# Kernel optimization log

Hardware: AMD Instinct MI355X
Metric: run time of the kernel (lower is better)

## Reference

```python
import jax, jax.numpy as jnp
import numpy as np

N = 256          # num agents
HID = 128        # hidden_dim
ACT = 5          # action_dim
NH = 4           # num_heads
D = HID + 16     # concat_hidden_dim = 144
E = D * NH       # mha embed dim = 576
HD = D           # per-head dim = E // NH = 144
OBS_RX, OBS_RY = 4, 2   # obs_r from fov_size=(9,5)
GRID = 40


def setup_inputs() -> dict:
    key = jax.random.key(0)
    ks = jax.random.split(key, 24)
    g = lambda k, shape, s: (jax.random.normal(k, shape, dtype=jnp.float32) * s)
    inp = {
        "hidden_state_n": g(ks[0], (N, HID), 1.0),
        "action_n": g(ks[1], (N, HID), 1.0),
        "state_n": jax.random.randint(ks[2], (N, 2), 0, GRID, dtype=jnp.int32),
        # obs encoder
        "W_enc": g(ks[3], (HID, 16), HID ** -0.5), "b_enc": jnp.zeros((16,), jnp.float32),
        # MHABlock outer projections
        "Wq": g(ks[4], (D, E), D ** -0.5), "bq": jnp.zeros((E,), jnp.float32),
        "Wk": g(ks[5], (D, E), D ** -0.5), "bk": jnp.zeros((E,), jnp.float32),
        "Wv": g(ks[6], (D, E), D ** -0.5), "bv": jnp.zeros((E,), jnp.float32),
        # nn.MultiheadAttention internal in/out projections
        "Wiq": g(ks[7], (E, E), E ** -0.5), "biq": jnp.zeros((E,), jnp.float32),
        "Wik": g(ks[8], (E, E), E ** -0.5), "bik": jnp.zeros((E,), jnp.float32),
        "Wiv": g(ks[9], (E, E), E ** -0.5), "biv": jnp.zeros((E,), jnp.float32),
        "Wo_proj": g(ks[10], (E, E), E ** -0.5), "bo_proj": jnp.zeros((E,), jnp.float32),
        "W_O": g(ks[11], (E, D), E ** -0.5),  # no bias
        # dueling decoders
        "W_val": g(ks[12], (D, 1), D ** -0.5), "b_val": jnp.zeros((1,), jnp.float32),
        "W_adv": g(ks[13], (D, ACT), D ** -0.5), "b_adv": jnp.zeros((ACT,), jnp.float32),
    }
    return inp


def reference(hidden_state_n, action_n, W_enc, b_enc, Wq, bq, Wk, bk, Wv, bv,
              Wiq, biq, Wik, bik, Wiv, biv, Wo_proj, bo_proj, W_O,
              W_val, b_val, W_adv, b_adv, state_n):
    n = hidden_state_n.shape[0]
    # observed_agents[i] = {j > i : |x_i-x_j|<=rx and |y_i-y_j|<=ry}
    pos = state_n.astype(jnp.int32)
    dx = jnp.abs(pos[:, None, 0] - pos[None, :, 0])
    dy = jnp.abs(pos[:, None, 1] - pos[None, :, 1])
    upper = jnp.arange(n)[None, :] > jnp.arange(n)[:, None]
    mask = (dx <= OBS_RX) & (dy <= OBS_RY) & upper            # [N,N], mask[i,j]: j observed by i

    # per-neighbor feature c_j = concat(obs_encoder(h_j), a_j)  -> [N, D]
    obs = hidden_state_n @ W_enc + b_enc                       # [N,16]
    C = jnp.concatenate([obs, action_n], axis=-1)              # [N,D]

    # MHABlock: outer Q/K/V projections then nn.MultiheadAttention
    q = (C @ Wq + bq) @ Wiq + biq                              # [N,E]
    k = (C @ Wk + bk) @ Wik + bik
    v = (C @ Wv + bv) @ Wiv + biv
    q2 = q.reshape(n, NH, HD)
    k2 = k.reshape(n, NH, HD)
    v2 = v.reshape(n, NH, HD)

    scale = 1.0 / np.sqrt(HD).astype(np.float32)
    S = jnp.einsum("jhd,khd->hjk", q2, k2) * scale             # [H,N,N] shared across agents

    pair = (mask[:, None, :, None] & mask[:, None, None, :])   # [N,1,Nq,Nk]
    logits = jnp.where(pair, S[None, :, :, :], -1e9)           # [N,H,N,N]
    m = jnp.max(logits, axis=-1, keepdims=True)
    p = jnp.exp(logits - m) * pair.astype(logits.dtype)
    attn = p / jnp.maximum(p.sum(axis=-1, keepdims=True), 1e-9)

    ctx = jnp.einsum("ihjk,khd->ijhd", attn, v2).reshape(n, n, E)  # [N,Nq,E]
    out = (ctx @ Wo_proj + bo_proj) @ W_O                          # [N,Nq,D]

    # sum over the (masked) neighbor/query axis -> per-agent h_i
    h = jnp.sum(out * mask[:, :, None].astype(out.dtype), axis=1)  # [N,D]

    V = h @ W_val + b_val                                          # [N,1]
    A = h @ W_adv + b_adv                                          # [N,ACT]
    Q = V + A - jnp.mean(A, axis=-1, keepdims=True)                # dueling Q
    return Q
```

## Files before the change

kernel.cpp:

```cpp
#include <hip/hip_runtime.h>

#define NAG 256
#define HID 128
#define ACT 5
#define NH 4
#define DD 144
#define EE 576
#define HDIM 144
#define CMAX 20

__device__ __forceinline__ void prod_tile24(
    const float* __restrict__ A, const float* __restrict__ W,
    float* __restrict__ out, int rowbase, int colbase, int N,
    int tid, float* __restrict__ sm)
{
    const int LDA = 580;
    float* As = sm;
    for (int idx = tid; idx < 24 * 144; idx += 256) {
        int r = idx / 144, c = idx % 144;
        *((float4*)&As[r * LDA + c * 4]) =
            *(const float4*)(A + (size_t)(rowbase + r) * 576 + c * 4);
    }
    __syncthreads();
    const int wave = tid >> 6, lane = tid & 63;
    const int colg = colbase + lane;
    const int colc = (colg < N) ? colg : (N - 1);
    const float* Wp = W + (size_t)(wave * 144) * N + colc;
    float acc[24] = {};
    float wv[24], wn[24];
    #pragma unroll
    for (int j = 0; j < 24; ++j) wv[j] = Wp[(size_t)j * N];
    for (int gi = 0; gi < 6; ++gi) {
        if (gi + 1 < 6) {
            const float* Wn = Wp + (size_t)(gi + 1) * 24 * N;
            #pragma unroll
            for (int j = 0; j < 24; ++j) wn[j] = Wn[(size_t)j * N];
        }
        const int kb = wave * 144 + gi * 24;
        #pragma unroll
        for (int j4 = 0; j4 < 6; ++j4) {
            #pragma unroll
            for (int r = 0; r < 24; ++r) {
                float4 a4 = *(const float4*)&As[r * LDA + kb + j4 * 4];
                acc[r] += a4.x * wv[j4 * 4 + 0] + a4.y * wv[j4 * 4 + 1]
                        + a4.z * wv[j4 * 4 + 2] + a4.w * wv[j4 * 4 + 3];
            }
        }
        #pragma unroll
        for (int j = 0; j < 24; ++j) wv[j] = wn[j];
    }
    __syncthreads();
    float* red = sm;
    #pragma unroll
    for (int r = 0; r < 24; ++r) red[wave * 1536 + r * 64 + lane] = acc[r];
    __syncthreads();
    #pragma unroll
    for (int qq = 0; qq < 6; ++qq) {
        int idx = tid + qq * 256;
        int r = idx >> 6, cl = idx & 63;
        int col = colbase + cl;
        if (col < N) {
            float s = red[idx] + red[1536 + idx] + red[3072 + idx] + red[4608 + idx];
            out[(size_t)(rowbase + r) * N + col] = s;
        }
    }
}

__global__ __launch_bounds__(256) void k_pre(
    const float* __restrict__ hidden, const float* __restrict__ action,
    const float* __restrict__ W_enc, const float* __restrict__ b_enc,
    const float* __restrict__ Wq, const float* __restrict__ Wk, const float* __restrict__ Wv,
    const float* __restrict__ bq, const float* __restrict__ bk, const float* __restrict__ bv,
    const float* __restrict__ Wiq, const float* __restrict__ Wik, const float* __restrict__ Wiv,
    const float* __restrict__ biq, const float* __restrict__ bik, const float* __restrict__ biv,
    const float* __restrict__ Wo, const float* __restrict__ bo, const float* __restrict__ W_O,
    float* __restrict__ C,
    float* __restrict__ Wqc, float* __restrict__ Wkc, float* __restrict__ Wvc,
    float* __restrict__ Wc,
    float* __restrict__ bqc, float* __restrict__ bkc, float* __restrict__ bvc,
    float* __restrict__ bvec)
{
    __shared__ float sm[13920];
    const int p = blockIdx.x, tid = threadIdx.x;
    if (p < 162) {
        const int g = p / 6, mt = p % 6;
        const int z = g / 9, bx = g % 9;
        const float* A = (z == 0) ? Wq  : (z == 1) ? Wk  : Wv;
        const float* W = (z == 0) ? Wiq : (z == 1) ? Wik : Wiv;
        float*     out = (z == 0) ? Wqc : (z == 1) ? Wkc : Wvc;
        prod_tile24(A, W, out, mt * 24, bx * 64, EE, tid, sm);
    } else if (p < 234) {
        const int t = p - 162;
        const int mt = t / 3, bx = t % 3;
        prod_tile24(Wo, W_O, Wc, mt * 24, bx * 64, DD, tid, sm);
    } else if (p < 266) {
        const int mb = p - 234;
        float* Hs = sm;
        float* We = sm + 1056;
        {
            int r = tid >> 5, kq = tid & 31;
            *((float4*)&Hs[r * 132 + kq * 4]) =
                *(const float4*)(hidden + (mb * 8 + r) * HID + kq * 4);
            float4 a4 = *(const float4*)(action + (mb * 8 + r) * HID + kq * 4);
            *((float4*)(C + (size_t)(mb * 8 + r) * DD + 16 + kq * 4)) = a4;
            *((float4*)&We[tid * 4])        = *(const float4*)(W_enc + tid * 4);
            *((float4*)&We[1024 + tid * 4]) = *(const float4*)(W_enc + 1024 + tid * 4);
        }
        __syncthreads();
        if (tid < 128) {
            int r = tid >> 4, o = tid & 15;
            float acc = 0.f;
            #pragma unroll 8
            for (int d = 0; d < HID; ++d) acc += Hs[r * 132 + d] * We[d * 16 + o];
            C[(size_t)(mb * 8 + r) * DD + o] = acc + b_enc[o];
        }
    } else {
        const int t = p - 266;
        const float *bsel, *W, *badd;
        float* out;
        int N, bx;
        if (t < 27) {
            int z = t / 9; bx = t % 9; N = EE;
            bsel = (z == 0) ? bq  : (z == 1) ? bk  : bv;
            W    = (z == 0) ? Wiq : (z == 1) ? Wik : Wiv;
            badd = (z == 0) ? biq : (z == 1) ? bik : biv;
            out  = (z == 0) ? bqc : (z == 1) ? bkc : bvc;
        } else {
            bx = t - 27; N = DD;
            bsel = bo; W = W_O; badd = nullptr; out = bvec;
        }
        float* bs = sm;
        float* red = sm + 576;
        for (int i = tid; i < 144; i += 256)
            *((float4*)&bs[i * 4]) = *(const float4*)(bsel + i * 4);
        __syncthreads();
        const int wave = tid >> 6, lane = tid & 63;
        const int colg = bx * 64 + lane;
        const int colc = (colg < N) ? colg : (N - 1);
        float acc = 0.f;
        for (int k = wave * 144; k < wave * 144 + 144; ++k)
            acc += bs[k] * W[(size_t)k * N + colc];
        red[wave * 64 + lane] = acc;
        __syncthreads();
        if (tid < 64 && bx * 64 + tid < N) {
            float s = red[tid] + red[64 + tid] + red[128 + tid] + red[192 + tid];
            out[bx * 64 + tid] = s + (badd ? badd[bx * 64 + tid] : 0.f);
        }
    }
}

__global__ __launch_bounds__(256) void k_qkv(
    const float* __restrict__ C,
    const float* __restrict__ Wqc, const float* __restrict__ Wkc, const float* __restrict__ Wvc,
    const float* __restrict__ bqc, const float* __restrict__ bkc, const float* __restrict__ bvc,
    float* __restrict__ q, float* __restrict__ kb, float* __restrict__ v)
{
    const int p = blockIdx.x;
    const int xcd = p & 7, qq = p >> 3;
    const int mb = qq & 31, gslot = qq >> 5;
    const int g = xcd + 8 * gslot;
    if (g >= 27) return;
    const int bx = g % 9, z = g / 9;
    const float* W  = (z == 0) ? Wqc : (z == 1) ? Wkc : Wvc;
    const float* bi = (z == 0) ? bqc : (z == 1) ? bkc : bvc;
    float*      out = (z == 0) ? q   : (z == 1) ? kb  : v;
    const int tid = threadIdx.x;

    __shared__ union { float As[8 * 148]; float red[2048]; } u;
    for (int idx = tid; idx < 8 * 36; idx += 256) {
        int r = idx / 36, c = idx % 36;
        *((float4*)&u.As[r * 148 + c * 4]) =
            *(const float4*)(C + (size_t)(mb * 8 + r) * DD + c * 4);
    }
    __syncthreads();
    const int wave = tid >> 6, lane = tid & 63;
    const int colg = bx * 64 + lane;
    const float* Wp = W + (size_t)(wave * 36) * EE + colg;
    float acc[8] = {};
    float wv[36];
    #pragma unroll
    for (int j = 0; j < 36; ++j) wv[j] = Wp[(size_t)j * EE];
    const int kbase = wave * 36;
    #pragma unroll
    for (int j4 = 0; j4 < 9; ++j4) {
        #pragma unroll
        for (int r = 0; r < 8; ++r) {
            float4 a4 = *(const float4*)&u.As[r * 148 + kbase + j4 * 4];
            acc[r] += a4.x * wv[j4 * 4 + 0] + a4.y * wv[j4 * 4 + 1]
                    + a4.z * wv[j4 * 4 + 2] + a4.w * wv[j4 * 4 + 3];
        }
    }
    __syncthreads();
    #pragma unroll
    for (int r = 0; r < 8; ++r) u.red[wave * 512 + r * 64 + lane] = acc[r];
    __syncthreads();
    #pragma unroll
    for (int qi = 0; qi < 2; ++qi) {
        int idx = tid + qi * 256;
        int r = idx >> 6, cl = idx & 63;
        int col = bx * 64 + cl;
        float s = u.red[idx] + u.red[512 + idx]
                + u.red[1024 + idx] + u.red[1536 + idx];
        out[(size_t)(mb * 8 + r) * EE + col] = s + bi[col];
    }
}

__global__ __launch_bounds__(256) void k_attn(
    const int* __restrict__ state, const float* __restrict__ q,
    const float* __restrict__ kmat, const float* __restrict__ v,
    float* __restrict__ ctxsum, float* __restrict__ cnt)
{
    __shared__ int lst[NAG];
    __shared__ int cnt_s;
    __shared__ float w4[NH][NAG];
    __shared__ float qh[CMAX][HDIM + 1];
    __shared__ float kh[CMAX][HDIM + 1];
    __shared__ float Sl[CMAX][CMAX + 1];
    const int i = blockIdx.x, tid = threadIdx.x;
    if (tid == 0) cnt_s = 0;
    __syncthreads();
    {
        int xi = state[2 * i], yi = state[2 * i + 1];
        int xj = state[2 * tid], yj = state[2 * tid + 1];
        int dx = xi - xj; if (dx < 0) dx = -dx;
        int dy = yi - yj; if (dy < 0) dy = -dy;
        if (tid > i && dx <= 4 && dy <= 2) {
            int p = atomicAdd(&cnt_s, 1);
            lst[p] = tid;
        }
    }
    __syncthreads();
    const int c = cnt_s;
    if (tid == 0) cnt[i] = (float)c;
    if (c == 0) {
        for (int e = tid; e < EE; e += 256) ctxsum[i * EE + e] = 0.f;
        return;
    }
    if (c <= CMAX) {
        for (int h = 0; h < NH; ++h) {
            for (int idx = tid; idx < c * HDIM; idx += 256) {
                int jj = idx / HDIM, d = idx % HDIM;
                qh[jj][d] = q[lst[jj] * EE + h * HDIM + d];
                kh[jj][d] = kmat[lst[jj] * EE + h * HDIM + d];
            }
            __syncthreads();
            for (int pp = tid; pp < c * c; pp += 256) {
                int jj = pp / c, kk = pp % c;
                float acc = 0.f;
                for (int d = 0; d < HDIM; ++d) acc += qh[jj][d] * kh[kk][d];
                Sl[jj][kk] = acc * (1.0f / 12.0f);
            }
            __syncthreads();
            if (tid < c) {
                float m = -1e30f;
                for (int kk = 0; kk < c; ++kk) m = fmaxf(m, Sl[tid][kk]);
                float zz = 0.f;
                for (int kk = 0; kk < c; ++kk) zz += __expf(Sl[tid][kk] - m);
                float inv = 1.f / fmaxf(zz, 1e-9f);
                for (int kk = 0; kk < c; ++kk)
                    Sl[tid][kk] = __expf(Sl[tid][kk] - m) * inv;
            }
            __syncthreads();
            if (tid < c) {
                float s = 0.f;
                for (int jj = 0; jj < c; ++jj) s += Sl[jj][tid];
                w4[h][tid] = s;
            }
            __syncthreads();
        }
    } else {
        for (int idx = tid; idx < NH * c; idx += 256) w4[idx / c][idx % c] = 0.f;
        __syncthreads();
        for (int pnh = tid; pnh < NH * c; pnh += 256) {
            int h = pnh / c, jj = pnh % c;
            const float* qrow = q + lst[jj] * EE + h * HDIM;
            float m = -1e30f;
            for (int kk = 0; kk < c; ++kk) {
                const float* krow = kmat + lst[kk] * EE + h * HDIM;
                float a = 0.f;
                for (int d = 0; d < HDIM; ++d) a += qrow[d] * krow[d];
                m = fmaxf(m, a * (1.0f / 12.0f));
            }
            float zz = 0.f;
            for (int kk = 0; kk < c; ++kk) {
                const float* krow = kmat + lst[kk] * EE + h * HDIM;
                float a = 0.f;
                for (int d = 0; d < HDIM; ++d) a += qrow[d] * krow[d];
                zz += __expf(a * (1.0f / 12.0f) - m);
            }
            float inv = 1.f / fmaxf(zz, 1e-9f);
            for (int kk = 0; kk < c; ++kk) {
                const float* krow = kmat + lst[kk] * EE + h * HDIM;
                float a = 0.f;
                for (int d = 0; d < HDIM; ++d) a += qrow[d] * krow[d];
                atomicAdd(&w4[h][kk], __expf(a * (1.0f / 12.0f) - m) * inv);
            }
        }
        __syncthreads();
    }
    for (int e = tid; e < EE; e += 256) {
        int h = e / HDIM;
        float a0 = 0.f, a1 = 0.f;
        int t = 0;
        for (; t + 1 < c; t += 2) {
            a0 += w4[h][t] * v[lst[t] * EE + e];
            a1 += w4[h][t + 1] * v[lst[t + 1] * EE + e];
        }
        if (t < c) a0 += w4[h][t] * v[lst[t] * EE + e];
        ctxsum[i * EE + e] = a0 + a1;
    }
}

__global__ __launch_bounds__(256) void k_tail(
    const float* __restrict__ ctx, const float* __restrict__ Wc,
    const float* __restrict__ cnt, const float* __restrict__ bvec,
    const float* __restrict__ W_val, const float* __restrict__ b_val,
    const float* __restrict__ W_adv, const float* __restrict__ b_adv,
    float* __restrict__ out)
{
    __shared__ float As[8][EE];
    __shared__ float hb[8][DD];
    const int b = blockIdx.x, tid = threadIdx.x;
    const int a0 = b * 8;
    for (int idx = tid; idx < 8 * (EE / 4); idx += 256) {
        int r = idx / (EE / 4), c4 = idx % (EE / 4);
        *((float4*)&As[r][c4 * 4]) =
            *(const float4*)(ctx + (size_t)(a0 + r) * EE + c4 * 4);
    }
    __syncthreads();
    if (tid < DD) {
        const int col = tid;
        const float* Wp = Wc + col;
        float ac[8] = {};
        float wv[32], wn[32];
        #pragma unroll
        for (int j = 0; j < 32; ++j) wv[j] = Wp[(size_t)j * DD];
        for (int gI = 0; gI < 18; ++gI) {
            if (gI + 1 < 18) {
                const float* Wn = Wp + (size_t)(gI + 1) * 32 * DD;
                #pragma unroll
                for (int j = 0; j < 32; ++j) wn[j] = Wn[(size_t)j * DD];
            }
            const int kbase = gI * 32;
            #pragma unroll
            for (int j = 0; j < 32; ++j) {
                float w = wv[j];
                #pragma unroll
                for (int s = 0; s < 8; ++s) ac[s] += As[s][kbase + j] * w;
            }
            #pragma unroll
            for (int j = 0; j < 32; ++j) wv[j] = wn[j];
        }
        float bvc = bvec[col];
        #pragma unroll
        for (int s = 0; s < 8; ++s) hb[s][col] = ac[s] + cnt[a0 + s] * bvc;
    }
    __syncthreads();
    const int wave = tid >> 6, lane = tid & 63;
    for (int s = 0; s < 2; ++s) {
        const int ag = wave * 2 + s;
        float h0 = hb[ag][lane], h1 = hb[ag][lane + 64];
        float h2 = (lane < 16) ? hb[ag][lane + 128] : 0.f;
        float red[6];
        for (int o = 0; o < 6; ++o) {
            float p;
            if (o < 5) {
                p = h0 * W_adv[lane * ACT + o] + h1 * W_adv[(lane + 64) * ACT + o];
                if (lane < 16) p += h2 * W_adv[(lane + 128) * ACT + o];
            } else {
                p = h0 * W_val[lane] + h1 * W_val[lane + 64];
                if (lane < 16) p += h2 * W_val[lane + 128];
            }
            for (int off = 32; off; off >>= 1) p += __shfl_xor(p, off);
            red[o] = p;
        }
        if (lane == 0) {
            float a[ACT], mean = 0.f;
            for (int o = 0; o < ACT; ++o) { a[o] = red[o] + b_adv[o]; mean += a[o]; }
            mean *= (1.0f / ACT);
            float V = red[5] + b_val[0];
            for (int o = 0; o < ACT; ++o) out[(a0 + ag) * ACT + o] = V + a[o] - mean;
        }
    }
}

extern "C" void kernel_launch(void* const* d_in, const int* in_sizes, int n_in,
                              void* d_out, int out_size, void* d_ws, size_t ws_size,
                              hipStream_t stream)
{
    const float* hidden = (const float*)d_in[0];
    const float* action = (const float*)d_in[1];
    const int*   state  = (const int*)d_in[2];

    float* ws = (float*)d_ws;
    float* C    = ws;
    float* Wqc  = C    + NAG * DD;
    float* Wkc  = Wqc  + DD * EE;
    float* Wvc  = Wkc  + DD * EE;
    float* Wc   = Wvc  + DD * EE;
    float* bqc  = Wc   + EE * DD;
    float* bkc  = bqc  + EE;
    float* bvc  = bkc  + EE;
    float* bvec = bvc  + EE;
    float* q    = bvec + DD;
    float* kb   = q    + NAG * EE;
    float* v    = kb   + NAG * EE;
    float* ctx  = v    + NAG * EE;
    float* cnt  = ctx  + NAG * EE;

    k_pre<<<296, 256, 0, stream>>>(hidden, action,
        (const float*)d_in[3], (const float*)d_in[4],
        (const float*)d_in[5], (const float*)d_in[7], (const float*)d_in[9],
        (const float*)d_in[6], (const float*)d_in[8], (const float*)d_in[10],
        (const float*)d_in[11], (const float*)d_in[13], (const float*)d_in[15],
        (const float*)d_in[12], (const float*)d_in[14], (const float*)d_in[16],
        (const float*)d_in[17], (const float*)d_in[18], (const float*)d_in[19],
        C, Wqc, Wkc, Wvc, Wc, bqc, bkc, bvc, bvec);

    k_qkv<<<1024, 256, 0, stream>>>(C, Wqc, Wkc, Wvc, bqc, bkc, bvc, q, kb, v);

    k_attn<<<NAG, 256, 0, stream>>>(state, q, kb, v, ctx, cnt);

    k_tail<<<32, 256, 0, stream>>>(ctx, Wc, cnt, bvec,
        (const float*)d_in[20], (const float*)d_in[21],
        (const float*)d_in[22], (const float*)d_in[23], (float*)d_out);
}
```

Baseline: 193.7 us.

## Drop weight-product precompute; apply chained projections directly per row tile

Removes the k_pre kernel that multiplied weight matrices together (Wq·Wiq, Wo·W_O) and folded biases. Instead, k_qkv computes the obs encoder, then the outer projection and then the inner projection for each 8-row tile, keeping the intermediate in shared memory. k_tail now applies Wo_proj and W_O in sequence on 2 agents per block. This saves a kernel launch and the large weight-by-weight GEMMs (about 3×144×576×576 FLOPs), but each block now re-reads full weight matrices, the QKV stage has far fewer blocks, and the outer projection is recomputed by each of the three column-slice blocks.

```diff
diff --git a/kernel.cpp b/kernel.cpp
--- a/kernel.cpp
+++ b/kernel.cpp
@@ -9,199 +9,126 @@
 #define HDIM 144
 #define CMAX 20
 
-__device__ __forceinline__ void prod_tile24(
-    const float* __restrict__ A, const float* __restrict__ W,
-    float* __restrict__ out, int rowbase, int colbase, int N,
-    int tid, float* __restrict__ sm)
-{
-    const int LDA = 580;
-    float* As = sm;
-    for (int idx = tid; idx < 24 * 144; idx += 256) {
-        int r = idx / 144, c = idx % 144;
-        *((float4*)&As[r * LDA + c * 4]) =
-            *(const float4*)(A + (size_t)(rowbase + r) * 576 + c * 4);
-    }
-    __syncthreads();
-    const int wave = tid >> 6, lane = tid & 63;
-    const int colg = colbase + lane;
-    const int colc = (colg < N) ? colg : (N - 1);
-    const float* Wp = W + (size_t)(wave * 144) * N + colc;
-    float acc[24] = {};
-    float wv[24], wn[24];
-    #pragma unroll
-    for (int j = 0; j < 24; ++j) wv[j] = Wp[(size_t)j * N];
-    for (int gi = 0; gi < 6; ++gi) {
-        if (gi + 1 < 6) {
-            const float* Wn = Wp + (size_t)(gi + 1) * 24 * N;
-            #pragma unroll
-            for (int j = 0; j < 24; ++j) wn[j] = Wn[(size_t)j * N];
-        }
-        const int kb = wave * 144 + gi * 24;
-        #pragma unroll
-        for (int j4 = 0; j4 < 6; ++j4) {
-            #pragma unroll
-            for (int r = 0; r < 24; ++r) {
-                float4 a4 = *(const float4*)&As[r * LDA + kb + j4 * 4];
-                acc[r] += a4.x * wv[j4 * 4 + 0] + a4.y * wv[j4 * 4 + 1]
-                        + a4.z * wv[j4 * 4 + 2] + a4.w * wv[j4 * 4 + 3];
-            }
-        }
-        #pragma unroll
-        for (int j = 0; j < 24; ++j) wv[j] = wn[j];
-    }
-    __syncthreads();
-    float* red = sm;
-    #pragma unroll
-    for (int r = 0; r < 24; ++r) red[wave * 1536 + r * 64 + lane] = acc[r];
-    __syncthreads();
-    #pragma unroll
-    for (int qq = 0; qq < 6; ++qq) {
-        int idx = tid + qq * 256;
-        int r = idx >> 6, cl = idx & 63;
-        int col = colbase + cl;
-        if (col < N) {
-            float s = red[idx] + red[1536 + idx] + red[3072 + idx] + red[4608 + idx];
-            out[(size_t)(rowbase + r) * N + col] = s;
-        }
-    }
-}
-
-__global__ __launch_bounds__(256) void k_pre(
+__global__ __launch_bounds__(256) void k_qkv(
     const float* __restrict__ hidden, const float* __restrict__ action,
     const float* __restrict__ W_enc, const float* __restrict__ b_enc,
-    const float* __restrict__ Wq, const float* __restrict__ Wk, const float* __restrict__ Wv,
-    const float* __restrict__ bq, const float* __restrict__ bk, const float* __restrict__ bv,
-    const float* __restrict__ Wiq, const float* __restrict__ Wik, const float* __restrict__ Wiv,
-    const float* __restrict__ biq, const float* __restrict__ bik, const float* __restrict__ biv,
-    const float* __restrict__ Wo, const float* __restrict__ bo, const float* __restrict__ W_O,
-    float* __restrict__ C,
-    float* __restrict__ Wqc, float* __restrict__ Wkc, float* __restrict__ Wvc,
-    float* __restrict__ Wc,
-    float* __restrict__ bqc, float* __restrict__ bkc, float* __restrict__ bvc,
-    float* __restrict__ bvec)
-{
-    __shared__ float sm[13920];
-    const int p = blockIdx.x, tid = threadIdx.x;
-    if (p < 162) {
-        const int g = p / 6, mt = p % 6;
-        const int z = g / 9, bx = g % 9;
-        const float* A = (z == 0) ? Wq  : (z == 1) ? Wk  : Wv;
-        const float* W = (z == 0) ? Wiq : (z == 1) ? Wik : Wiv;
-        float*     out = (z == 0) ? Wqc : (z == 1) ? Wkc : Wvc;
-        prod_tile24(A, W, out, mt * 24, bx * 64, EE, tid, sm);
-    } else if (p < 234) {
-        const int t = p - 162;
-        const int mt = t / 3, bx = t % 3;
-        prod_tile24(Wo, W_O, Wc, mt * 24, bx * 64, DD, tid, sm);
-    } else if (p < 266) {
-        const int mb = p - 234;
-        float* Hs = sm;
-        float* We = sm + 1056;
-        {
-            int r = tid >> 5, kq = tid & 31;
-            *((float4*)&Hs[r * 132 + kq * 4]) =
-                *(const float4*)(hidden + (mb * 8 + r) * HID + kq * 4);
-            float4 a4 = *(const float4*)(action + (mb * 8 + r) * HID + kq * 4);
-            *((float4*)(C + (size_t)(mb * 8 + r) * DD + 16 + kq * 4)) = a4;
-            *((float4*)&We[tid * 4])        = *(const float4*)(W_enc + tid * 4);
-            *((float4*)&We[1024 + tid * 4]) = *(const float4*)(W_enc + 1024 + tid * 4);
-        }
-        __syncthreads();
-        if (tid < 128) {
-            int r = tid >> 4, o = tid & 15;
-            float acc = 0.f;
-            #pragma unroll 8
-            for (int d = 0; d < HID; ++d) acc += Hs[r * 132 + d] * We[d * 16 + o];
-            C[(size_t)(mb * 8 + r) * DD + o] = acc + b_enc[o];
-        }
-    } else {
-        const int t = p - 266;
-        const float *bsel, *W, *badd;
-        float* out;
-        int N, bx;
-        if (t < 27) {
-            int z = t / 9; bx = t % 9; N = EE;
-            bsel = (z == 0) ? bq  : (z == 1) ? bk  : bv;
-            W    = (z == 0) ? Wiq : (z == 1) ? Wik : Wiv;
-            badd = (z == 0) ? biq : (z == 1) ? bik : biv;
-            out  = (z == 0) ? bqc : (z == 1) ? bkc : bvc;
-        } else {
-            bx = t - 27; N = DD;
-            bsel = bo; W = W_O; badd = nullptr; out = bvec;
-        }
-        float* bs = sm;
-        float* red = sm + 576;
-        for (int i = tid; i < 144; i += 256)
-            *((float4*)&bs[i * 4]) = *(const float4*)(bsel + i * 4);
-        __syncthreads();
-        const int wave = tid >> 6, lane = tid & 63;
-        const int colg = bx * 64 + lane;
-        const int colc = (colg < N) ? colg : (N - 1);
-        float acc = 0.f;
-        for (int k = wave * 144; k < wave * 144 + 144; ++k)
-            acc += bs[k] * W[(size_t)k * N + colc];
-        red[wave * 64 + lane] = acc;
-        __syncthreads();
-        if (tid < 64 && bx * 64 + tid < N) {
-            float s = red[tid] + red[64 + tid] + red[128 + tid] + red[192 + tid];
-            out[bx * 64 + tid] = s + (badd ? badd[bx * 64 + tid] : 0.f);
-        }
-    }
-}
-
-__global__ __launch_bounds__(256) void k_qkv(
-    const float* __restrict__ C,
-    const float* __restrict__ Wqc, const float* __restrict__ Wkc, const float* __restrict__ Wvc,
-    const float* __restrict__ bqc, const float* __restrict__ bkc, const float* __restrict__ bvc,
+    const float* __restrict__ Wq, const float* __restrict__ bq,
+    const float* __restrict__ Wiq, const float* __restrict__ biq,
+    const float* __restrict__ Wk, const float* __restrict__ bk,
+    const float* __restrict__ Wik, const float* __restrict__ bik,
+    const float* __restrict__ Wv, const float* __restrict__ bv,
+    const float* __restrict__ Wiv, const float* __restrict__ biv,
     float* __restrict__ q, float* __restrict__ kb, float* __restrict__ v)
 {
-    const int p = blockIdx.x;
-    const int xcd = p & 7, qq = p >> 3;
-    const int mb = qq & 31, gslot = qq >> 5;
-    const int g = xcd + 8 * gslot;
-    if (g >= 27) return;
-    const int bx = g % 9, z = g / 9;
-    const float* W  = (z == 0) ? Wqc : (z == 1) ? Wkc : Wvc;
-    const float* bi = (z == 0) ? bqc : (z == 1) ? bkc : bvc;
-    float*      out = (z == 0) ? q   : (z == 1) ? kb  : v;
-    const int tid = threadIdx.x;
-
-    __shared__ union { float As[8 * 148]; float red[2048]; } u;
-    for (int idx = tid; idx < 8 * 36; idx += 256) {
-        int r = idx / 36, c = idx % 36;
-        *((float4*)&u.As[r * 148 + c * 4]) =
-            *(const float4*)(C + (size_t)(mb * 8 + r) * DD + c * 4);
-    }
-    __syncthreads();
-    const int wave = tid >> 6, lane = tid & 63;
-    const int colg = bx * 64 + lane;
-    const float* Wp = W + (size_t)(wave * 36) * EE + colg;
-    float acc[8] = {};
-    float wv[36];
-    #pragma unroll
-    for (int j = 0; j < 36; ++j) wv[j] = Wp[(size_t)j * EE];
-    const int kbase = wave * 36;
-    #pragma unroll
-    for (int j4 = 0; j4 < 9; ++j4) {
+    __shared__ float Hs[8 * 132];
+    __shared__ float We[2048];
+    __shared__ float C8[8 * 148];
+    __shared__ float T8[8 * 580];
+    const int p = blockIdx.x, tid = threadIdx.x;
+    const int mt = p & 31, zc = p >> 5;
+    const int z = zc / 3, cs = zc % 3;
+    const float* Wz = (z == 0) ? Wq  : (z == 1) ? Wk  : Wv;
+    const float* bz = (z == 0) ? bq  : (z == 1) ? bk  : bv;
+    const float* Wi = (z == 0) ? Wiq : (z == 1) ? Wik : Wiv;
+    const float* bi = (z == 0) ? biq : (z == 1) ? bik : biv;
+    float*     outp = (z == 0) ? q   : (z == 1) ? kb  : v;
+    const int row0 = mt * 8;
+
+    {
+        int r = tid >> 5, k4 = tid & 31;
+        *((float4*)&Hs[r * 132 + k4 * 4]) =
+            *(const float4*)(hidden + (size_t)(row0 + r) * HID + k4 * 4);
+        *((float4*)&C8[r * 148 + 16 + k4 * 4]) =
+            *(const float4*)(action + (size_t)(row0 + r) * HID + k4 * 4);
+        *((float4*)&We[tid * 4])        = *(const float4*)(W_enc + tid * 4);
+        *((float4*)&We[1024 + tid * 4]) = *(const float4*)(W_enc + 1024 + tid * 4);
+    }
+    __syncthreads();
+    if (tid < 128) {
+        int r = tid >> 4, o = tid & 15;
+        float acc = 0.f;
+        #pragma unroll 8
+        for (int d = 0; d < HID; ++d) acc += Hs[r * 132 + d] * We[d * 16 + o];
+        C8[r * 148 + o] = acc + b_enc[o];
+    }
+    __syncthreads();
+
+    {
+        const int c0 = tid, c1 = tid + 256, c2 = tid + 512;
+        const bool has2 = (tid < 64);
+        float a0[8] = {}, a1[8] = {}, a2[8] = {};
+        float w0[8], w1[8], w2[8], n0[8], n1[8], n2[8];
+        #pragma unroll
+        for (int j = 0; j < 8; ++j) {
+            w0[j] = Wz[(size_t)j * EE + c0];
+            w1[j] = Wz[(size_t)j * EE + c1];
+            w2[j] = has2 ? Wz[(size_t)j * EE + c2] : 0.f;
+        }
+        for (int g = 0; g < 18; ++g) {
+            if (g + 1 < 18) {
+                const float* Wn = Wz + (size_t)(g + 1) * 8 * EE;
+                #pragma unroll
+                for (int j = 0; j < 8; ++j) {
+                    n0[j] = Wn[(size_t)j * EE + c0];
+                    n1[j] = Wn[(size_t)j * EE + c1];
+                    n2[j] = has2 ? Wn[(size_t)j * EE + c2] : 0.f;
+                }
+            }
+            const int kb0 = g * 8;
+            #pragma unroll
+            for (int j4 = 0; j4 < 2; ++j4) {
+                #pragma unroll
+                for (int r = 0; r < 8; ++r) {
+                    float4 cv = *((const float4*)&C8[r * 148 + kb0 + j4 * 4]);
+                    const int j = j4 * 4;
+                    a0[r] += cv.x * w0[j] + cv.y * w0[j + 1] + cv.z * w0[j + 2] + cv.w * w0[j + 3];
+                    a1[r] += cv.x * w1[j] + cv.y * w1[j + 1] + cv.z * w1[j + 2] + cv.w * w1[j + 3];
+                    a2[r] += cv.x * w2[j] + cv.y * w2[j + 1] + cv.z * w2[j + 2] + cv.w * w2[j + 3];
+                }
+            }
+            #pragma unroll
+            for (int j = 0; j < 8; ++j) { w0[j] = n0[j]; w1[j] = n1[j]; w2[j] = n2[j]; }
+        }
+        float b0 = bz[c0], b1 = bz[c1], b2 = has2 ? bz[c2] : 0.f;
         #pragma unroll
         for (int r = 0; r < 8; ++r) {
-            float4 a4 = *(const float4*)&u.As[r * 148 + kbase + j4 * 4];
-            acc[r] += a4.x * wv[j4 * 4 + 0] + a4.y * wv[j4 * 4 + 1]
-                    + a4.z * wv[j4 * 4 + 2] + a4.w * wv[j4 * 4 + 3];
-        }
-    }
-    __syncthreads();
-    #pragma unroll
-    for (int r = 0; r < 8; ++r) u.red[wave * 512 + r * 64 + lane] = acc[r];
-    __syncthreads();
-    #pragma unroll
-    for (int qi = 0; qi < 2; ++qi) {
-        int idx = tid + qi * 256;
-        int r = idx >> 6, cl = idx & 63;
-        int col = bx * 64 + cl;
-        float s = u.red[idx] + u.red[512 + idx]
-                + u.red[1024 + idx] + u.red[1536 + idx];
-        out[(size_t)(mb * 8 + r) * EE + col] = s + bi[col];
+            T8[r * 580 + c0] = a0[r] + b0;
+            T8[r * 580 + c1] = a1[r] + b1;
+            if (has2) T8[r * 580 + c2] = a2[r] + b2;
+        }
+    }
+    __syncthreads();
+
+    if (tid < 192) {
+        const int col = cs * 192 + tid;
+        float acc[8] = {};
+        float wv[16], wn[16];
+        const float* Wp = Wi + col;
+        #pragma unroll
+        for (int j = 0; j < 16; ++j) wv[j] = Wp[(size_t)j * EE];
+        for (int g = 0; g < 36; ++g) {
+            if (g + 1 < 36) {
+                const float* Wn = Wp + (size_t)(g + 1) * 16 * EE;
+                #pragma unroll
+                for (int j = 0; j < 16; ++j) wn[j] = Wn[(size_t)j * EE];
+            }
+            const int kb0 = g * 16;
+            #pragma unroll
+            for (int j4 = 0; j4 < 4; ++j4) {
+                #pragma unroll
+                for (int r = 0; r < 8; ++r) {
+                    float4 tv = *((const float4*)&T8[r * 580 + kb0 + j4 * 4]);
+                    const int j = j4 * 4;
+                    acc[r] += tv.x * wv[j] + tv.y * wv[j + 1] + tv.z * wv[j + 2] + tv.w * wv[j + 3];
+                }
+            }
+            #pragma unroll
+            for (int j = 0; j < 16; ++j) wv[j] = wn[j];
+        }
+        const float bic = bi[col];
+        #pragma unroll
+        for (int r = 0; r < 8; ++r)
+            outp[(size_t)(row0 + r) * EE + col] = acc[r] + bic;
     }
 }
 
@@ -312,64 +239,119 @@
 }
 
 __global__ __launch_bounds__(256) void k_tail(
-    const float* __restrict__ ctx, const float* __restrict__ Wc,
-    const float* __restrict__ cnt, const float* __restrict__ bvec,
+    const float* __restrict__ ctx, const float* __restrict__ cnt,
+    const float* __restrict__ Wo, const float* __restrict__ bo,
+    const float* __restrict__ W_O,
     const float* __restrict__ W_val, const float* __restrict__ b_val,
     const float* __restrict__ W_adv, const float* __restrict__ b_adv,
     float* __restrict__ out)
 {
-    __shared__ float As[8][EE];
-    __shared__ float hb[8][DD];
+    __shared__ float c2[2 * 580];
+    __shared__ float g2[2 * 580];
+    __shared__ float h2[2 * DD];
     const int b = blockIdx.x, tid = threadIdx.x;
-    const int a0 = b * 8;
-    for (int idx = tid; idx < 8 * (EE / 4); idx += 256) {
-        int r = idx / (EE / 4), c4 = idx % (EE / 4);
-        *((float4*)&As[r][c4 * 4]) =
-            *(const float4*)(ctx + (size_t)(a0 + r) * EE + c4 * 4);
-    }
-    __syncthreads();
+    const int a0 = b * 2;
+    for (int idx = tid; idx < 2 * (EE / 4); idx += 256) {
+        int a = idx / (EE / 4), k4 = idx % (EE / 4);
+        *((float4*)&c2[a * 580 + k4 * 4]) =
+            *(const float4*)(ctx + (size_t)(a0 + a) * EE + k4 * 4);
+    }
+    __syncthreads();
+
+    {
+        const int c0 = tid, c1 = tid + 256, cc2 = tid + 512;
+        const bool has2 = (tid < 64);
+        float a00 = 0.f, a01 = 0.f, a02 = 0.f;
+        float a10 = 0.f, a11 = 0.f, a12 = 0.f;
+        float w0[8], w1[8], w2[8], n0[8], n1[8], n2[8];
+        #pragma unroll
+        for (int j = 0; j < 8; ++j) {
+            w0[j] = Wo[(size_t)j * EE + c0];
+            w1[j] = Wo[(size_t)j * EE + c1];
+            w2[j] = has2 ? Wo[(size_t)j * EE + cc2] : 0.f;
+        }
+        for (int g = 0; g < 72; ++g) {
+            if (g + 1 < 72) {
+                const float* Wn = Wo + (size_t)(g + 1) * 8 * EE;
+                #pragma unroll
+                for (int j = 0; j < 8; ++j) {
+                    n0[j] = Wn[(size_t)j * EE + c0];
+                    n1[j] = Wn[(size_t)j * EE + c1];
+                    n2[j] = has2 ? Wn[(size_t)j * EE + cc2] : 0.f;
+                }
+            }
+            const int kb0 = g * 8;
+            #pragma unroll
+            for (int j4 = 0; j4 < 2; ++j4) {
+                float4 x0 = *((const float4*)&c2[0 * 580 + kb0 + j4 * 4]);
+                float4 x1 = *((const float4*)&c2[1 * 580 + kb0 + j4 * 4]);
+                const int j = j4 * 4;
+                a00 += x0.x * w0[j] + x0.y * w0[j + 1] + x0.z * w0[j + 2] + x0.w * w0[j + 3];
+                a01 += x0.x * w1[j] + x0.y * w1[j + 1] + x0.z * w1[j + 2] + x0.w * w1[j + 3];
+                a02 += x0.x * w2[j] + x0.y * w2[j + 1] + x0.z * w2[j + 2] + x0.w * w2[j + 3];
+                a10 += x1.x * w0[j] + x1.y * w0[j + 1] + x1.z * w0[j + 2] + x1.w * w0[j + 3];
+                a11 += x1.x * w1[j] + x1.y * w1[j + 1] + x1.z * w1[j + 2] + x1.w * w1[j + 3];
+                a12 += x1.x * w2[j] + x1.y * w2[j + 1] + x1.z * w2[j + 2] + x1.w * w2[j + 3];
+            }
+            #pragma unroll
+            for (int j = 0; j < 8; ++j) { w0[j] = n0[j]; w1[j] = n1[j]; w2[j] = n2[j]; }
+        }
+        const float ct0 = cnt[a0], ct1 = cnt[a0 + 1];
+        g2[0 * 580 + c0] = a00 + ct0 * bo[c0];
+        g2[1 * 580 + c0] = a10 + ct1 * bo[c0];
+        g2[0 * 580 + c1] = a01 + ct0 * bo[c1];
+        g2[1 * 580 + c1] = a11 + ct1 * bo[c1];
+        if (has2) {
+            g2[0 * 580 + cc2] = a02 + ct0 * bo[cc2];
+            g2[1 * 580 + cc2] = a12 + ct1 * bo[cc2];
+        }
+    }
+    __syncthreads();
+
     if (tid < DD) {
         const int col = tid;
-        const float* Wp = Wc + col;
-        float ac[8] = {};
-        float wv[32], wn[32];
-        #pragma unroll
-        for (int j = 0; j < 32; ++j) wv[j] = Wp[(size_t)j * DD];
-        for (int gI = 0; gI < 18; ++gI) {
-            if (gI + 1 < 18) {
-                const float* Wn = Wp + (size_t)(gI + 1) * 32 * DD;
-                #pragma unroll
-                for (int j = 0; j < 32; ++j) wn[j] = Wn[(size_t)j * DD];
-            }
-            const int kbase = gI * 32;
-            #pragma unroll
-            for (int j = 0; j < 32; ++j) {
-                float w = wv[j];
-                #pragma unroll
-                for (int s = 0; s < 8; ++s) ac[s] += As[s][kbase + j] * w;
-            }
-            #pragma unroll
-            for (int j = 0; j < 32; ++j) wv[j] = wn[j];
-        }
-        float bvc = bvec[col];
-        #pragma unroll
-        for (int s = 0; s < 8; ++s) hb[s][col] = ac[s] + cnt[a0 + s] * bvc;
-    }
-    __syncthreads();
+        float ac0 = 0.f, ac1 = 0.f;
+        float wv[8], wn[8];
+        const float* Wp = W_O + col;
+        #pragma unroll
+        for (int j = 0; j < 8; ++j) wv[j] = Wp[(size_t)j * DD];
+        for (int g = 0; g < 72; ++g) {
+            if (g + 1 < 72) {
+                const float* Wn = Wp + (size_t)(g + 1) * 8 * DD;
+                #pragma unroll
+                for (int j = 0; j < 8; ++j) wn[j] = Wn[(size_t)j * DD];
+            }
+            const int kb0 = g * 8;
+            #pragma unroll
+            for (int j4 = 0; j4 < 2; ++j4) {
+                float4 x0 = *((const float4*)&g2[0 * 580 + kb0 + j4 * 4]);
+                float4 x1 = *((const float4*)&g2[1 * 580 + kb0 + j4 * 4]);
+                const int j = j4 * 4;
+                ac0 += x0.x * wv[j] + x0.y * wv[j + 1] + x0.z * wv[j + 2] + x0.w * wv[j + 3];
+                ac1 += x1.x * wv[j] + x1.y * wv[j + 1] + x1.z * wv[j + 2] + x1.w * wv[j + 3];
+            }
+            #pragma unroll
+            for (int j = 0; j < 8; ++j) wv[j] = wn[j];
+        }
+        h2[0 * DD + col] = ac0;
+        h2[1 * DD + col] = ac1;
+    }
+    __syncthreads();
+
     const int wave = tid >> 6, lane = tid & 63;
-    for (int s = 0; s < 2; ++s) {
-        const int ag = wave * 2 + s;
-        float h0 = hb[ag][lane], h1 = hb[ag][lane + 64];
-        float h2 = (lane < 16) ? hb[ag][lane + 128] : 0.f;
+    if (wave < 2) {
+        const int ag = wave;
+        float h0 = h2[ag * DD + lane], h1 = h2[ag * DD + lane + 64];
+        float hh2 = (lane < 16) ? h2[ag * DD + lane + 128] : 0.f;
         float red[6];
         for (int o = 0; o < 6; ++o) {
             float p;
             if (o < 5) {
                 p = h0 * W_adv[lane * ACT + o] + h1 * W_adv[(lane + 64) * ACT + o];
-                if (lane < 16) p += h2 * W_adv[(lane + 128) * ACT + o];
+                if (lane < 16) p += hh2 * W_adv[(lane + 128) * ACT + o];
             } else {
                 p = h0 * W_val[lane] + h1 * W_val[lane + 64];
-                if (lane < 16) p += h2 * W_val[lane + 128];
+                if (lane < 16) p += hh2 * W_val[lane + 128];
             }
             for (int off = 32; off; off >>= 1) p += __shfl_xor(p, off);
             red[o] = p;
@@ -393,35 +375,26 @@
     const int*   state  = (const int*)d_in[2];
 
     float* ws = (float*)d_ws;
-    float* C    = ws;
-    float* Wqc  = C    + NAG * DD;
-    float* Wkc  = Wqc  + DD * EE;
-    float* Wvc  = Wkc  + DD * EE;
-    float* Wc   = Wvc  + DD * EE;
-    float* bqc  = Wc   + EE * DD;
-    float* bkc  = bqc  + EE;
-    float* bvc  = bkc  + EE;
-    float* bvec = bvc  + EE;
-    float* q    = bvec + DD;
-    float* kb   = q    + NAG * EE;
-    float* v    = kb   + NAG * EE;
-    float* ctx  = v    + NAG * EE;
-    float* cnt  = ctx  + NAG * EE;
-
-    k_pre<<<296, 256, 0, stream>>>(hidden, action,
+    float* q    = ws;
+    float* kb   = q   + NAG * EE;
+    float* v    = kb  + NAG * EE;
+    float* ctx  = v   + NAG * EE;
+    float* cnt  = ctx + NAG * EE;
+
+    k_qkv<<<288, 256, 0, stream>>>(hidden, action,
         (const float*)d_in[3], (const float*)d_in[4],
-        (const float*)d_in[5], (const float*)d_in[7], (const float*)d_in[9],
-        (const float*)d_in[6], (const float*)d_in[8], (const float*)d_in[10],
-        (const float*)d_in[11], (const float*)d_in[13], (const float*)d_in[15],
-        (const float*)d_in[12], (const float*)d_in[14], (const float*)d_in[16],
+        (const float*)d_in[5], (const float*)d_in[6],
+        (const float*)d_in[11], (const float*)d_in[12],
+        (const float*)d_in[7], (const float*)d_in[8],
+        (const float*)d_in[13], (const float*)d_in[14],
+        (const float*)d_in[9], (const float*)d_in[10],
+        (const float*)d_in[15], (const float*)d_in[16],
+        q, kb, v);
+
+    k_attn<<<NAG, 256, 0, stream>>>(state, q, kb, v, ctx, cnt);
+
+    k_tail<<<128, 256, 0, stream>>>(ctx, cnt,
         (const float*)d_in[17], (const float*)d_in[18], (const float*)d_in[19],
-        C, Wqc, Wkc, Wvc, Wc, bqc, bkc, bvc, bvec);
-
-    k_qkv<<<1024, 256, 0, stream>>>(C, Wqc, Wkc, Wvc, bqc, bkc, bvc, q, kb, v);
-
-    k_attn<<<NAG, 256, 0, stream>>>(state, q, kb, v, ctx, cnt);
-
-    k_tail<<<32, 256, 0, stream>>>(ctx, Wc, cnt, bvec,
         (const float*)d_in[20], (const float*)d_in[21],
         (const float*)d_in[22], (const float*)d_in[23], (float*)d_out);
 }
```

Result: slower. 246.8 us (+27.4%).
